# Kernel optimization log

Measured on AMD Instinct MI355X. Metric: run time of the kernel, lower is better.

## Reference

```python
import jax, jax.numpy as jnp
import numpy as np

B, C, H, W = 16, 1024, 32, 32


def setup_inputs() -> dict:
    key = jax.random.key(0)
    ka, kb, kc = jax.random.split(key, 3)
    a = jax.random.normal(ka, (B, C, H, W), dtype=jnp.float32)
    b = jax.random.normal(kb, (B, C, H, W), dtype=jnp.float32)
    c = jax.random.normal(kc, (B, C, H, W), dtype=jnp.float32)
    return {"a": a, "b": b, "c": c}


def reference(a, b, c):
    Bn, Cn = a.shape[0], a.shape[1]
    a_f = a.reshape(Bn, Cn, -1)  # [B, C, HW]
    b_f = b.reshape(Bn, Cn, -1)
    c_f = c.reshape(Bn, Cn, -1)
    # channel-attention scores: [B, C, C]
    scores = jnp.einsum('bik,bjk->bij', b_f, c_f)
    mid = jax.nn.softmax(scores, axis=-1)
    out = jnp.einsum('bij,bjk->bik', mid, a_f)  # [B, C, HW]
    out = out.reshape(a.shape) + a  # residual add
    return out
```

## Files before the change

kernel.cpp:

```cpp
#include <hip/hip_runtime.h>
#include <hip/hip_bf16.h>
#include <stdint.h>

#define BATCH 16
#define CDIM 1024
#define HWDIM 1024
#define PSTRIDE 2048

typedef __bf16 bf16_t;
typedef short short8 __attribute__((ext_vector_type(8)));
typedef float floatx4 __attribute__((ext_vector_type(4)));

__global__ __launch_bounds__(256) void k_gemm1(const float* __restrict__ Bm,
                                               const float* __restrict__ Cm,
                                               float* __restrict__ S) {
    const int bz = blockIdx.z;
    const int i0 = blockIdx.x * 128;
    const int j0 = blockIdx.y * 128;
    const float* Ap = Bm + (size_t)bz * CDIM * HWDIM;
    const float* Bp = Cm + (size_t)bz * CDIM * HWDIM;
    float* Sp = S + (size_t)bz * CDIM * CDIM;

    __shared__ bf16_t lAhi[128 * 32], lAlo[128 * 32];
    __shared__ bf16_t lBhi[128 * 32], lBlo[128 * 32];

    const int tid = threadIdx.x;
    const int lane = tid & 63;
    const int wave = tid >> 6;
    const int wm = wave >> 1, wn = wave & 1;

    floatx4 acc[4][4];
#pragma unroll
    for (int a = 0; a < 4; ++a)
#pragma unroll
        for (int b = 0; b < 4; ++b) acc[a][b] = (floatx4){0.f, 0.f, 0.f, 0.f};

    const int srow = tid >> 2;
    const int scol = (tid & 3) * 8;
    const int fr = lane & 15;
    const int fk = (lane >> 4) * 8;

    for (int k0 = 0; k0 < HWDIM; k0 += 32) {
#pragma unroll
        for (int p = 0; p < 2; ++p) {
            const int row = p * 64 + srow;
            {
                const float* g = Ap + (size_t)(i0 + row) * HWDIM + k0 + scol;
                bf16_t h[8], l[8];
#pragma unroll
                for (int e = 0; e < 8; ++e) {
                    float x = g[e];
                    __bf16 hh = (__bf16)x;
                    h[e] = hh;
                    l[e] = (__bf16)(x - (float)hh);
                }
                *(uint4*)&lAhi[row * 32 + scol] = *(const uint4*)h;
                *(uint4*)&lAlo[row * 32 + scol] = *(const uint4*)l;
            }
            {
                const float* g = Bp + (size_t)(j0 + row) * HWDIM + k0 + scol;
                bf16_t h[8], l[8];
#pragma unroll
                for (int e = 0; e < 8; ++e) {
                    float x = g[e];
                    __bf16 hh = (__bf16)x;
                    h[e] = hh;
                    l[e] = (__bf16)(x - (float)hh);
                }
                *(uint4*)&lBhi[row * 32 + scol] = *(const uint4*)h;
                *(uint4*)&lBlo[row * 32 + scol] = *(const uint4*)l;
            }
        }
        __syncthreads();
        short8 ah[4], al[4], bh[4], bl[4];
#pragma unroll
        for (int mt = 0; mt < 4; ++mt) {
            const int off = (wm * 64 + mt * 16 + fr) * 32 + fk;
            ah[mt] = *(const short8*)&lAhi[off];
            al[mt] = *(const short8*)&lAlo[off];
        }
#pragma unroll
        for (int nt = 0; nt < 4; ++nt) {
            const int off = (wn * 64 + nt * 16 + fr) * 32 + fk;
            bh[nt] = *(const short8*)&lBhi[off];
            bl[nt] = *(const short8*)&lBlo[off];
        }
#pragma unroll
        for (int mt = 0; mt < 4; ++mt)
#pragma unroll
            for (int nt = 0; nt < 4; ++nt) {
                acc[mt][nt] = __builtin_amdgcn_mfma_f32_16x16x32_bf16(
                    ah[mt], bh[nt], acc[mt][nt], 0, 0, 0);
                acc[mt][nt] = __builtin_amdgcn_mfma_f32_16x16x32_bf16(
                    ah[mt], bl[nt], acc[mt][nt], 0, 0, 0);
                acc[mt][nt] = __builtin_amdgcn_mfma_f32_16x16x32_bf16(
                    al[mt], bh[nt], acc[mt][nt], 0, 0, 0);
            }
        __syncthreads();
    }

    const int er = (lane >> 4) * 4;
    const int ec = lane & 15;
#pragma unroll
    for (int mt = 0; mt < 4; ++mt)
#pragma unroll
        for (int nt = 0; nt < 4; ++nt) {
            const int row = i0 + wm * 64 + mt * 16 + er;
            const int col = j0 + wn * 64 + nt * 16 + ec;
            float* dst = Sp + (size_t)row * CDIM + col;
#pragma unroll
            for (int r = 0; r < 4; ++r) dst[(size_t)r * CDIM] = acc[mt][nt][r];
        }
}

__global__ __launch_bounds__(256) void k_softmax(float* __restrict__ S) {
    float* rp = S + (size_t)blockIdx.x * CDIM;
    const int tid = threadIdx.x;
    float4 v = ((const float4*)rp)[tid];

    __shared__ float red[256];
    float m = fmaxf(fmaxf(v.x, v.y), fmaxf(v.z, v.w));
    red[tid] = m;
    __syncthreads();
    for (int s = 128; s > 0; s >>= 1) {
        if (tid < s) red[tid] = fmaxf(red[tid], red[tid + s]);
        __syncthreads();
    }
    m = red[0];
    __syncthreads();

    float e0 = __expf(v.x - m), e1 = __expf(v.y - m);
    float e2 = __expf(v.z - m), e3 = __expf(v.w - m);
    red[tid] = e0 + e1 + e2 + e3;
    __syncthreads();
    for (int s = 128; s > 0; s >>= 1) {
        if (tid < s) red[tid] += red[tid + s];
        __syncthreads();
    }
    const float inv = 1.0f / red[0];

    bf16_t p[4];
    p[0] = (__bf16)(e0 * inv);
    p[1] = (__bf16)(e1 * inv);
    p[2] = (__bf16)(e2 * inv);
    p[3] = (__bf16)(e3 * inv);
    ((uint2*)rp)[tid] = *(const uint2*)p;
}

__global__ __launch_bounds__(256) void k_transpose(const float* __restrict__ A,
                                                   bf16_t* __restrict__ SP) {
    const int bz = blockIdx.z;
    const int t0 = blockIdx.x * 64;
    const int j0 = blockIdx.y * 64;
    const float* Ap = A + (size_t)bz * CDIM * HWDIM;
    bf16_t* Atp = SP + (size_t)bz * CDIM * PSTRIDE + 1024;

    __shared__ bf16_t tile[64][68];
    const int lr = threadIdx.x >> 4;
    const int lc = (threadIdx.x & 15) * 4;
#pragma unroll
    for (int r = 0; r < 4; ++r) {
        const float* src = Ap + (size_t)(j0 + lr + r * 16) * HWDIM + t0 + lc;
        float4 f = *(const float4*)src;
        bf16_t t4[4];
        t4[0] = (__bf16)f.x; t4[1] = (__bf16)f.y;
        t4[2] = (__bf16)f.z; t4[3] = (__bf16)f.w;
        *(uint2*)&tile[lr + r * 16][lc] = *(const uint2*)t4;
    }
    __syncthreads();
#pragma unroll
    for (int r = 0; r < 4; ++r) {
        const int trow = lr + r * 16;
        bf16_t tmp[4];
#pragma unroll
        for (int e = 0; e < 4; ++e) tmp[e] = tile[lc + e][trow];
        *(uint2*)(Atp + (size_t)(t0 + trow) * PSTRIDE + j0 + lc) = *(uint2*)tmp;
    }
}

__global__ __launch_bounds__(256) void k_gemm2(const bf16_t* __restrict__ SP,
                                               const float* __restrict__ Aorig,
                                               float* __restrict__ Out) {
    const int bz = blockIdx.z;
    const int i0 = blockIdx.x * 128;
    const int t0 = blockIdx.y * 128;
    const bf16_t* Pp = SP + (size_t)bz * CDIM * PSTRIDE;
    const bf16_t* Bp = SP + (size_t)bz * CDIM * PSTRIDE + 1024;

    __shared__ bf16_t lA[128 * 32];
    __shared__ bf16_t lB[128 * 32];

    const int tid = threadIdx.x;
    const int lane = tid & 63;
    const int wave = tid >> 6;
    const int wm = wave >> 1, wn = wave & 1;

    floatx4 acc[4][4];
#pragma unroll
    for (int a = 0; a < 4; ++a)
#pragma unroll
        for (int b = 0; b < 4; ++b) acc[a][b] = (floatx4){0.f, 0.f, 0.f, 0.f};

    const int srow = tid >> 2;
    const int scol = (tid & 3) * 8;
    const int fr = lane & 15;
    const int fk = (lane >> 4) * 8;

    for (int k0 = 0; k0 < CDIM; k0 += 32) {
        uint4 va[2], vb[2];
#pragma unroll
        for (int p = 0; p < 2; ++p) {
            va[p] = *(const uint4*)(Pp + (size_t)(i0 + p * 64 + srow) * PSTRIDE + k0 + scol);
            vb[p] = *(const uint4*)(Bp + (size_t)(t0 + p * 64 + srow) * PSTRIDE + k0 + scol);
        }
#pragma unroll
        for (int p = 0; p < 2; ++p) {
            *(uint4*)&lA[(p * 64 + srow) * 32 + scol] = va[p];
            *(uint4*)&lB[(p * 64 + srow) * 32 + scol] = vb[p];
        }
        __syncthreads();
        short8 af[4], bfr[4];
#pragma unroll
        for (int mt = 0; mt < 4; ++mt)
            af[mt] = *(const short8*)&lA[(wm * 64 + mt * 16 + fr) * 32 + fk];
#pragma unroll
        for (int nt = 0; nt < 4; ++nt)
            bfr[nt] = *(const short8*)&lB[(wn * 64 + nt * 16 + fr) * 32 + fk];
#pragma unroll
        for (int mt = 0; mt < 4; ++mt)
#pragma unroll
            for (int nt = 0; nt < 4; ++nt)
                acc[mt][nt] = __builtin_amdgcn_mfma_f32_16x16x32_bf16(
                    af[mt], bfr[nt], acc[mt][nt], 0, 0, 0);
        __syncthreads();
    }

    const float* ap = Aorig + (size_t)bz * CDIM * HWDIM;
    float* op = Out + (size_t)bz * CDIM * HWDIM;
    const int er = (lane >> 4) * 4;
    const int ec = lane & 15;
#pragma unroll
    for (int mt = 0; mt < 4; ++mt)
#pragma unroll
        for (int nt = 0; nt < 4; ++nt) {
            const int col = t0 + wn * 64 + nt * 16 + ec;
#pragma unroll
            for (int r = 0; r < 4; ++r) {
                const int row = i0 + wm * 64 + mt * 16 + er + r;
                const size_t idx = (size_t)row * HWDIM + col;
                op[idx] = acc[mt][nt][r] + ap[idx];
            }
        }
}

extern "C" void kernel_launch(void* const* d_in, const int* in_sizes, int n_in,
                              void* d_out, int out_size, void* d_ws, size_t ws_size,
                              hipStream_t stream) {
    const float* a = (const float*)d_in[0];
    const float* b = (const float*)d_in[1];
    const float* c = (const float*)d_in[2];
    float* out = (float*)d_out;

    float* S = (float*)d_ws;

    k_gemm1<<<dim3(8, 8, 16), 256, 0, stream>>>(b, c, S);
    k_softmax<<<dim3(BATCH * CDIM), 256, 0, stream>>>(S);
    k_transpose<<<dim3(16, 16, 16), 256, 0, stream>>>(a, (bf16_t*)S);
    k_gemm2<<<dim3(8, 8, 16), 256, 0, stream>>>((const bf16_t*)S, a, out);
}
```

Baseline: 386.7 us.

## Switch GEMMs to fp16 with a pre-conversion pass and direct global-to-LDS loads

Drops the split-bf16 (hi/lo, three MFMAs) emulation in the score GEMM. Instead, a separate prep kernel converts b and c to fp16 into the output buffer, and both GEMMs use a single fp16 MFMA per tile. Tile loads now go straight from global memory to LDS with global_load_lds, which skips the register staging. This cuts MFMA work and conversion in the inner loop, at the cost of an extra conversion pass and lower score precision, since fp16 scores of 1024-length dot products may lose accuracy or overflow.

```diff
diff --git a/kernel.cpp b/kernel.cpp
--- a/kernel.cpp
+++ b/kernel.cpp
@@ -7,22 +7,43 @@
 #define HWDIM 1024
 #define PSTRIDE 2048
 
-typedef __bf16 bf16_t;
-typedef short short8 __attribute__((ext_vector_type(8)));
+typedef _Float16 half_t;
+typedef _Float16 half8 __attribute__((ext_vector_type(8)));
 typedef float floatx4 __attribute__((ext_vector_type(4)));
 
-__global__ __launch_bounds__(256) void k_gemm1(const float* __restrict__ Bm,
-                                               const float* __restrict__ Cm,
+__device__ static inline void gld_lds16(const half_t* g, half_t* l) {
+    __builtin_amdgcn_global_load_lds(
+        (__attribute__((address_space(1))) void*)(void*)g,
+        (__attribute__((address_space(3))) void*)l, 16, 0, 0);
+}
+
+__global__ __launch_bounds__(256) void k_prep(const float* __restrict__ Bm,
+                                              const float* __restrict__ Cm,
+                                              half_t* __restrict__ dst) {
+    const size_t N = (size_t)BATCH * CDIM * HWDIM;
+    const float* src = blockIdx.y ? Cm : Bm;
+    half_t* d = dst + (size_t)blockIdx.y * N;
+    const size_t base = ((size_t)blockIdx.x * 256 + threadIdx.x) * 8;
+    float4 f0 = *(const float4*)(src + base);
+    float4 f1 = *(const float4*)(src + base + 4);
+    half_t h[8];
+    h[0] = (half_t)f0.x; h[1] = (half_t)f0.y; h[2] = (half_t)f0.z; h[3] = (half_t)f0.w;
+    h[4] = (half_t)f1.x; h[5] = (half_t)f1.y; h[6] = (half_t)f1.z; h[7] = (half_t)f1.w;
+    *(uint4*)(d + base) = *(const uint4*)h;
+}
+
+__global__ __launch_bounds__(256) void k_gemm1(const half_t* __restrict__ Bh,
+                                               const half_t* __restrict__ Ch,
                                                float* __restrict__ S) {
     const int bz = blockIdx.z;
     const int i0 = blockIdx.x * 128;
     const int j0 = blockIdx.y * 128;
-    const float* Ap = Bm + (size_t)bz * CDIM * HWDIM;
-    const float* Bp = Cm + (size_t)bz * CDIM * HWDIM;
+    const half_t* Ap = Bh + (size_t)bz * CDIM * HWDIM;
+    const half_t* Bp = Ch + (size_t)bz * CDIM * HWDIM;
     float* Sp = S + (size_t)bz * CDIM * CDIM;
 
-    __shared__ bf16_t lAhi[128 * 32], lAlo[128 * 32];
-    __shared__ bf16_t lBhi[128 * 32], lBlo[128 * 32];
+    __shared__ half_t lA[128 * 32];
+    __shared__ half_t lB[128 * 32];
 
     const int tid = threadIdx.x;
     const int lane = tid & 63;
@@ -43,59 +64,25 @@
     for (int k0 = 0; k0 < HWDIM; k0 += 32) {
 #pragma unroll
         for (int p = 0; p < 2; ++p) {
-            const int row = p * 64 + srow;
-            {
-                const float* g = Ap + (size_t)(i0 + row) * HWDIM + k0 + scol;
-                bf16_t h[8], l[8];
-#pragma unroll
-                for (int e = 0; e < 8; ++e) {
-                    float x = g[e];
-                    __bf16 hh = (__bf16)x;
-                    h[e] = hh;
-                    l[e] = (__bf16)(x - (float)hh);
-                }
-                *(uint4*)&lAhi[row * 32 + scol] = *(const uint4*)h;
-                *(uint4*)&lAlo[row * 32 + scol] = *(const uint4*)l;
-            }
-            {
-                const float* g = Bp + (size_t)(j0 + row) * HWDIM + k0 + scol;
-                bf16_t h[8], l[8];
-#pragma unroll
-                for (int e = 0; e < 8; ++e) {
-                    float x = g[e];
-                    __bf16 hh = (__bf16)x;
-                    h[e] = hh;
-                    l[e] = (__bf16)(x - (float)hh);
-                }
-                *(uint4*)&lBhi[row * 32 + scol] = *(const uint4*)h;
-                *(uint4*)&lBlo[row * 32 + scol] = *(const uint4*)l;
-            }
-        }
-        __syncthreads();
-        short8 ah[4], al[4], bh[4], bl[4];
-#pragma unroll
-        for (int mt = 0; mt < 4; ++mt) {
-            const int off = (wm * 64 + mt * 16 + fr) * 32 + fk;
-            ah[mt] = *(const short8*)&lAhi[off];
-            al[mt] = *(const short8*)&lAlo[off];
-        }
-#pragma unroll
-        for (int nt = 0; nt < 4; ++nt) {
-            const int off = (wn * 64 + nt * 16 + fr) * 32 + fk;
-            bh[nt] = *(const short8*)&lBhi[off];
-            bl[nt] = *(const short8*)&lBlo[off];
-        }
-#pragma unroll
-        for (int mt = 0; mt < 4; ++mt)
-#pragma unroll
-            for (int nt = 0; nt < 4; ++nt) {
-                acc[mt][nt] = __builtin_amdgcn_mfma_f32_16x16x32_bf16(
-                    ah[mt], bh[nt], acc[mt][nt], 0, 0, 0);
-                acc[mt][nt] = __builtin_amdgcn_mfma_f32_16x16x32_bf16(
-                    ah[mt], bl[nt], acc[mt][nt], 0, 0, 0);
-                acc[mt][nt] = __builtin_amdgcn_mfma_f32_16x16x32_bf16(
-                    al[mt], bh[nt], acc[mt][nt], 0, 0, 0);
-            }
+            gld_lds16(Ap + (size_t)(i0 + p * 64 + srow) * HWDIM + k0 + scol,
+                      &lA[(p * 64 + srow) * 32 + scol]);
+            gld_lds16(Bp + (size_t)(j0 + p * 64 + srow) * HWDIM + k0 + scol,
+                      &lB[(p * 64 + srow) * 32 + scol]);
+        }
+        __syncthreads();
+        half8 af[4], bfr[4];
+#pragma unroll
+        for (int mt = 0; mt < 4; ++mt)
+            af[mt] = *(const half8*)&lA[(wm * 64 + mt * 16 + fr) * 32 + fk];
+#pragma unroll
+        for (int nt = 0; nt < 4; ++nt)
+            bfr[nt] = *(const half8*)&lB[(wn * 64 + nt * 16 + fr) * 32 + fk];
+#pragma unroll
+        for (int mt = 0; mt < 4; ++mt)
+#pragma unroll
+            for (int nt = 0; nt < 4; ++nt)
+                acc[mt][nt] = __builtin_amdgcn_mfma_f32_16x16x32_f16(
+                    af[mt], bfr[nt], acc[mt][nt], 0, 0, 0);
         __syncthreads();
     }
 
@@ -139,56 +126,56 @@
     }
     const float inv = 1.0f / red[0];
 
-    bf16_t p[4];
-    p[0] = (__bf16)(e0 * inv);
-    p[1] = (__bf16)(e1 * inv);
-    p[2] = (__bf16)(e2 * inv);
-    p[3] = (__bf16)(e3 * inv);
+    half_t p[4];
+    p[0] = (half_t)(e0 * inv);
+    p[1] = (half_t)(e1 * inv);
+    p[2] = (half_t)(e2 * inv);
+    p[3] = (half_t)(e3 * inv);
     ((uint2*)rp)[tid] = *(const uint2*)p;
 }
 
 __global__ __launch_bounds__(256) void k_transpose(const float* __restrict__ A,
-                                                   bf16_t* __restrict__ SP) {
+                                                   half_t* __restrict__ SP) {
     const int bz = blockIdx.z;
     const int t0 = blockIdx.x * 64;
     const int j0 = blockIdx.y * 64;
     const float* Ap = A + (size_t)bz * CDIM * HWDIM;
-    bf16_t* Atp = SP + (size_t)bz * CDIM * PSTRIDE + 1024;
-
-    __shared__ bf16_t tile[64][68];
+    half_t* Atp = SP + (size_t)bz * CDIM * PSTRIDE + 1024;
+
+    __shared__ half_t tile[64][68];
     const int lr = threadIdx.x >> 4;
     const int lc = (threadIdx.x & 15) * 4;
 #pragma unroll
     for (int r = 0; r < 4; ++r) {
         const float* src = Ap + (size_t)(j0 + lr + r * 16) * HWDIM + t0 + lc;
         float4 f = *(const float4*)src;
-        bf16_t t4[4];
-        t4[0] = (__bf16)f.x; t4[1] = (__bf16)f.y;
-        t4[2] = (__bf16)f.z; t4[3] = (__bf16)f.w;
+        half_t t4[4];
+        t4[0] = (half_t)f.x; t4[1] = (half_t)f.y;
+        t4[2] = (half_t)f.z; t4[3] = (half_t)f.w;
         *(uint2*)&tile[lr + r * 16][lc] = *(const uint2*)t4;
     }
     __syncthreads();
 #pragma unroll
     for (int r = 0; r < 4; ++r) {
         const int trow = lr + r * 16;
-        bf16_t tmp[4];
+        half_t tmp[4];
 #pragma unroll
         for (int e = 0; e < 4; ++e) tmp[e] = tile[lc + e][trow];
         *(uint2*)(Atp + (size_t)(t0 + trow) * PSTRIDE + j0 + lc) = *(uint2*)tmp;
     }
 }
 
-__global__ __launch_bounds__(256) void k_gemm2(const bf16_t* __restrict__ SP,
+__global__ __launch_bounds__(256) void k_gemm2(const half_t* __restrict__ SP,
                                                const float* __restrict__ Aorig,
                                                float* __restrict__ Out) {
     const int bz = blockIdx.z;
     const int i0 = blockIdx.x * 128;
     const int t0 = blockIdx.y * 128;
-    const bf16_t* Pp = SP + (size_t)bz * CDIM * PSTRIDE;
-    const bf16_t* Bp = SP + (size_t)bz * CDIM * PSTRIDE + 1024;
-
-    __shared__ bf16_t lA[128 * 32];
-    __shared__ bf16_t lB[128 * 32];
+    const half_t* Pp = SP + (size_t)bz * CDIM * PSTRIDE;
+    const half_t* Bp = SP + (size_t)bz * CDIM * PSTRIDE + 1024;
+
+    __shared__ half_t lA[128 * 32];
+    __shared__ half_t lB[128 * 32];
 
     const int tid = threadIdx.x;
     const int lane = tid & 63;
@@ -207,30 +194,26 @@
     const int fk = (lane >> 4) * 8;
 
     for (int k0 = 0; k0 < CDIM; k0 += 32) {
-        uint4 va[2], vb[2];
 #pragma unroll
         for (int p = 0; p < 2; ++p) {
-            va[p] = *(const uint4*)(Pp + (size_t)(i0 + p * 64 + srow) * PSTRIDE + k0 + scol);
-            vb[p] = *(const uint4*)(Bp + (size_t)(t0 + p * 64 + srow) * PSTRIDE + k0 + scol);
-        }
-#pragma unroll
-        for (int p = 0; p < 2; ++p) {
-            *(uint4*)&lA[(p * 64 + srow) * 32 + scol] = va[p];
-            *(uint4*)&lB[(p * 64 + srow) * 32 + scol] = vb[p];
-        }
-        __syncthreads();
-        short8 af[4], bfr[4];
-#pragma unroll
-        for (int mt = 0; mt < 4; ++mt)
-            af[mt] = *(const short8*)&lA[(wm * 64 + mt * 16 + fr) * 32 + fk];
+            gld_lds16(Pp + (size_t)(i0 + p * 64 + srow) * PSTRIDE + k0 + scol,
+                      &lA[(p * 64 + srow) * 32 + scol]);
+            gld_lds16(Bp + (size_t)(t0 + p * 64 + srow) * PSTRIDE + k0 + scol,
+                      &lB[(p * 64 + srow) * 32 + scol]);
+        }
+        __syncthreads();
+        half8 af[4], bfr[4];
+#pragma unroll
+        for (int mt = 0; mt < 4; ++mt)
+            af[mt] = *(const half8*)&lA[(wm * 64 + mt * 16 + fr) * 32 + fk];
 #pragma unroll
         for (int nt = 0; nt < 4; ++nt)
-            bfr[nt] = *(const short8*)&lB[(wn * 64 + nt * 16 + fr) * 32 + fk];
+            bfr[nt] = *(const half8*)&lB[(wn * 64 + nt * 16 + fr) * 32 + fk];
 #pragma unroll
         for (int mt = 0; mt < 4; ++mt)
 #pragma unroll
             for (int nt = 0; nt < 4; ++nt)
-                acc[mt][nt] = __builtin_amdgcn_mfma_f32_16x16x32_bf16(
+                acc[mt][nt] = __builtin_amdgcn_mfma_f32_16x16x32_f16(
                     af[mt], bfr[nt], acc[mt][nt], 0, 0, 0);
         __syncthreads();
     }
@@ -262,9 +245,12 @@
     float* out = (float*)d_out;
 
     float* S = (float*)d_ws;
-
-    k_gemm1<<<dim3(8, 8, 16), 256, 0, stream>>>(b, c, S);
+    half_t* bc16 = (half_t*)d_out;
+
+    k_prep<<<dim3(8192, 2), 256, 0, stream>>>(b, c, bc16);
+    k_gemm1<<<dim3(8, 8, 16), 256, 0, stream>>>(
+        bc16, bc16 + (size_t)BATCH * CDIM * HWDIM, S);
     k_softmax<<<dim3(BATCH * CDIM), 256, 0, stream>>>(S);
-    k_transpose<<<dim3(16, 16, 16), 256, 0, stream>>>(a, (bf16_t*)S);
-    k_gemm2<<<dim3(8, 8, 16), 256, 0, stream>>>((const bf16_t*)S, a, out);
-}
+    k_transpose<<<dim3(16, 16, 16), 256, 0, stream>>>(a, (half_t*)S);
+    k_gemm2<<<dim3(8, 8, 16), 256, 0, stream>>>((const half_t*)S, a, out);
+}
```

New measurement: 356.0 us. 7.9% less time.
